# Kernel optimization log

Measured on AMD Instinct MI355X. Metric: run time of the kernel, lower is better.

Reference implementation:

```python
import jax, jax.numpy as jnp
import numpy as np

N_NODES = 50000
HIDDEN = 256
N_EDGES = 300000


def setup_inputs() -> dict:
    key = jax.random.key(0)
    k1, k2, k3, k4 = jax.random.split(key, 4)
    node_embeddings = jax.random.normal(k1, (N_NODES, HIDDEN), dtype=jnp.float32)
    edge_weights_index = jax.random.randint(k2, (2, N_EDGES), 0, N_NODES, dtype=jnp.int64)
    # lin1: Linear(2H -> H), lin2: Linear(H -> 1); jax convention [in, out]
    W1 = jax.random.normal(k3, (2 * HIDDEN, HIDDEN), dtype=jnp.float32) * (1.0 / np.sqrt(2 * HIDDEN))
    b1 = jnp.zeros((HIDDEN,), dtype=jnp.float32)
    W2 = jax.random.normal(k4, (HIDDEN, 1), dtype=jnp.float32) * (1.0 / np.sqrt(HIDDEN))
    b2 = jnp.zeros((1,), dtype=jnp.float32)
    return {"node_embeddings": node_embeddings, "edge_weights_index": edge_weights_index,
            "W1": W1, "b1": b1, "W2": W2, "b2": b2}


def reference(node_embeddings, edge_weights_index, W1, b1, W2, b2):
    src = edge_weights_index[0, :]
    trg = edge_weights_index[1, :]
    # Split W1 into src/trg halves: concat([s, t]) @ W1 == s @ W1s + t @ W1t.
    # Avoids materializing the [E, 2H] concatenated edge tensor.
    W1s, W1t = W1[:HIDDEN], W1[HIDDEN:]
    h = node_embeddings[src] @ W1s + node_embeddings[trg] @ W1t + b1  # [E, H]
    h = jax.nn.relu(h)
    prediction = h @ W2 + b2  # [E, 1]
    return prediction.reshape(-1)
```

## Files before the change

kernel.cpp:

```cpp
#include <hip/hip_runtime.h>
#include <hip/hip_bf16.h>

#define N_NODES 50000
#define HID     256
#define N_EDGES 300000
#define NT      32
#define NTILES  ((N_NODES + NT - 1) / NT)

typedef __attribute__((ext_vector_type(8))) short bf16x8;
typedef __attribute__((ext_vector_type(4))) float f32x4;

__device__ __forceinline__ unsigned short f2bf(float f) {
  unsigned int u = __float_as_uint(f);
  u = (u + 0x7FFFu + ((u >> 16) & 1u)) >> 16;
  return (unsigned short)u;
}
__device__ __forceinline__ float bflo(unsigned int u) { return __uint_as_float(u << 16); }
__device__ __forceinline__ float bfhi(unsigned int u) { return __uint_as_float(u & 0xFFFF0000u); }

__device__ __forceinline__ bf16x8 cvt8(float4 u, float4 v) {
  bf16x8 r;
  r[0] = (short)f2bf(u.x); r[1] = (short)f2bf(u.y);
  r[2] = (short)f2bf(u.z); r[3] = (short)f2bf(u.w);
  r[4] = (short)f2bf(v.x); r[5] = (short)f2bf(v.y);
  r[6] = (short)f2bf(v.z); r[7] = (short)f2bf(v.w);
  return r;
}

struct StageRegs { float4 a, b, c, d; };

__device__ __forceinline__ void load_tile(const float* __restrict__ E, int tile,
                                          int srow, int sg, StageRegs& s) {
  int grow = tile * NT + srow;
  if (grow < N_NODES) {
    const float4* p = reinterpret_cast<const float4*>(E + (size_t)grow * HID + sg * 8);
    s.a = p[0]; s.b = p[1]; s.c = p[32]; s.d = p[33];
  } else {
    s.a = s.b = s.c = s.d = make_float4(0.f, 0.f, 0.f, 0.f);
  }
}

__global__ __launch_bounds__(128) void pack_w_kernel(
    const float* __restrict__ W1, unsigned short* __restrict__ Wtf) {
  int k = blockIdx.x;
  int t = threadIdx.x;
  int half = t >> 6;
  int jj = (t & 63) * 4;
  const float4 v = *reinterpret_cast<const float4*>(
      W1 + (size_t)(half ? (HID + k) : k) * HID + jj);
  float vv[4] = {v.x, v.y, v.z, v.w};
#pragma unroll
  for (int e = 0; e < 4; ++e) {
    int j = half * HID + jj + e;
    int f    = (j >> 4) * 8 + (k >> 5);
    int lane = (j & 15) | (((k >> 3) & 3) << 4);
    int elem = k & 7;
    Wtf[f * 512 + lane * 8 + elem] = f2bf(vv[e]);
  }
}

__global__ __launch_bounds__(512, 2) void gemm_kernel(
    const float* __restrict__ E, const unsigned short* __restrict__ Wtf,
    const float* __restrict__ b1, unsigned short* __restrict__ P) {
  __shared__ alignas(16) char lds0[16384];
  __shared__ alignas(16) char lds1[16384];
  const int tid  = threadIdx.x;
  const int lane = tid & 63;
  const int w    = tid >> 6;

  bf16x8 a[4][8];
#pragma unroll
  for (int m = 0; m < 4; ++m)
#pragma unroll
    for (int kk = 0; kk < 8; ++kk)
      a[m][kk] = *reinterpret_cast<const bf16x8*>(
          Wtf + (((size_t)(w * 4 + m) * 8 + kk) << 9) + lane * 8);

  float4 bv[4];
#pragma unroll
  for (int m = 0; m < 4; ++m) {
    int fm = w * 4 + m;
    bv[m] = (fm < 16) ? *reinterpret_cast<const float4*>(b1 + fm * 16 + ((lane >> 4) << 2))
                      : make_float4(0.f, 0.f, 0.f, 0.f);
  }

  const int srow = tid >> 4;
  const int sg   = tid & 15;
  const int woff0 = srow * 512 + ((sg * 16) ^ ((srow & 7) << 4));
  const int woff1 = srow * 512 + (((sg + 16) * 16) ^ ((srow & 7) << 4));
  const int G = gridDim.x;

  auto write_tile = [&](char* buf, const StageRegs& s) {
    *reinterpret_cast<bf16x8*>(&buf[woff0]) = cvt8(s.a, s.b);
    *reinterpret_cast<bf16x8*>(&buf[woff1]) = cvt8(s.c, s.d);
  };

  auto compute_store = [&](const char* buf, int tt) {
    f32x4 acc[4][2] = {};
#pragma unroll
    for (int n = 0; n < 2; ++n) {
      int r   = n * 16 + (lane & 15);
      int rb  = r * 512;
      int sw  = (r & 7) << 4;
      int kb0 = (lane >> 4) << 4;
      bf16x8 bfr[8];
#pragma unroll
      for (int kk = 0; kk < 8; ++kk)
        bfr[kk] = *reinterpret_cast<const bf16x8*>(&buf[rb + ((kk * 64 + kb0) ^ sw)]);
#pragma unroll
      for (int kk = 0; kk < 8; ++kk)
#pragma unroll
        for (int m = 0; m < 4; ++m)
          acc[m][n] = __builtin_amdgcn_mfma_f32_16x16x32_bf16(a[m][kk], bfr[kk], acc[m][n], 0, 0, 0);
    }
#pragma unroll
    for (int m = 0; m < 4; ++m) {
      int pcb = (w * 4 + m) * 16 + ((lane >> 4) << 2);
#pragma unroll
      for (int n = 0; n < 2; ++n) {
        int node = tt * NT + n * 16 + (lane & 15);
        if (node < N_NODES) {
          ushort4 o;
          o.x = f2bf(acc[m][n][0] + bv[m].x);
          o.y = f2bf(acc[m][n][1] + bv[m].y);
          o.z = f2bf(acc[m][n][2] + bv[m].z);
          o.w = f2bf(acc[m][n][3] + bv[m].w);
          *reinterpret_cast<ushort4*>(P + (size_t)node * 512 + pcb) = o;
        }
      }
    }
  };

  int t = blockIdx.x;
  if (t >= NTILES) return;
  StageRegs sX, sY;
  load_tile(E, t, srow, sg, sX);
  if (t + G < NTILES) load_tile(E, t + G, srow, sg, sY);
  write_tile(lds0, sX);
  if (t + 2 * G < NTILES) load_tile(E, t + 2 * G, srow, sg, sX);
  __syncthreads();

  while (true) {
    if (t + G < NTILES) {
      write_tile(lds1, sY);
      if (t + 3 * G < NTILES) load_tile(E, t + 3 * G, srow, sg, sY);
    }
    compute_store(lds0, t);
    if (t + G >= NTILES) break;
    __syncthreads();
    t += G;
    if (t + G < NTILES) {
      write_tile(lds0, sX);
      if (t + 3 * G < NTILES) load_tile(E, t + 3 * G, srow, sg, sX);
    }
    compute_store(lds1, t);
    if (t + G >= NTILES) break;
    __syncthreads();
    t += G;
  }
}

__global__ __launch_bounds__(256) void edge_kernel(
    const int* __restrict__ idx, const unsigned short* __restrict__ P,
    const float* __restrict__ W2, const float* __restrict__ b2,
    float* __restrict__ out) {
  const int tid  = threadIdx.x;
  const int lane = tid & 63;
  const int l32  = lane & 31;
  const int half = lane >> 5;
  const int wv     = blockIdx.x * 4 + (tid >> 6);
  const int nwaves = gridDim.x * 4;
  const float4 w0 = *reinterpret_cast<const float4*>(W2 + l32 * 8);
  const float4 w1 = *reinterpret_cast<const float4*>(W2 + l32 * 8 + 4);
  const float bias = b2[0];
  for (int ep = wv; ep < N_EDGES / 2; ep += nwaves) {
    int e = ep * 2 + half;
    int s = idx[e];
    int t = idx[N_EDGES + e];
    uint4 ua = *reinterpret_cast<const uint4*>(P + (size_t)s * 512 + l32 * 8);
    uint4 ub = *reinterpret_cast<const uint4*>(P + (size_t)t * 512 + 256 + l32 * 8);
    float h0 = fmaxf(bflo(ua.x) + bflo(ub.x), 0.f);
    float h1 = fmaxf(bfhi(ua.x) + bfhi(ub.x), 0.f);
    float h2 = fmaxf(bflo(ua.y) + bflo(ub.y), 0.f);
    float h3 = fmaxf(bfhi(ua.y) + bfhi(ub.y), 0.f);
    float h4 = fmaxf(bflo(ua.z) + bflo(ub.z), 0.f);
    float h5 = fmaxf(bfhi(ua.z) + bfhi(ub.z), 0.f);
    float h6 = fmaxf(bflo(ua.w) + bflo(ub.w), 0.f);
    float h7 = fmaxf(bfhi(ua.w) + bfhi(ub.w), 0.f);
    float acc = h0 * w0.x + h1 * w0.y + h2 * w0.z + h3 * w0.w
              + h4 * w1.x + h5 * w1.y + h6 * w1.z + h7 * w1.w;
#pragma unroll
    for (int off = 1; off < 32; off <<= 1)
      acc += __shfl_xor(acc, off, 64);
    if (l32 == 0) out[e] = acc + bias;
  }
}

extern "C" void kernel_launch(void* const* d_in, const int* in_sizes, int n_in,
                              void* d_out, int out_size, void* d_ws, size_t ws_size,
                              hipStream_t stream) {
  const float* E   = (const float*)d_in[0];
  const int*   idx = (const int*)d_in[1];
  const float* W1  = (const float*)d_in[2];
  const float* b1  = (const float*)d_in[3];
  const float* W2  = (const float*)d_in[4];
  const float* b2  = (const float*)d_in[5];
  float* out = (float*)d_out;

  unsigned short* Wtf = (unsigned short*)d_ws;
  unsigned short* P   = (unsigned short*)((char*)d_ws + 262144);

  hipLaunchKernelGGL(pack_w_kernel, dim3(HID), dim3(128), 0, stream, W1, Wtf);
  hipLaunchKernelGGL(gemm_kernel, dim3(256), dim3(512), 0, stream, E, Wtf, b1, P);
  hipLaunchKernelGGL(edge_kernel, dim3(2048), dim3(256), 0, stream, idx, P, W2, b2, out);
}
```

Baseline: 78.54 us.

## Bucket edges by source node range to improve gather locality in edge kernel

Adds a three-kernel counting sort (histogram, scan, scatter) that bins edges by the high bits of the source node index and writes permuted (src, trg, edge id) records. A new edge kernel walks the sorted list with a swizzled block-to-chunk mapping so that source-row gathers from P hit nearby rows and reuse cache. The cost is three extra launches, a 300k-record scatter with atomics, and scattered output writes; it falls back to the old path if the workspace is too small.

```diff
diff --git a/kernel.cpp b/kernel.cpp
--- a/kernel.cpp
+++ b/kernel.cpp
@@ -6,6 +6,11 @@
 #define N_EDGES 300000
 #define NT      32
 #define NTILES  ((N_NODES + NT - 1) / NT)
+#define NBINS   64
+#define SBLK    128
+#define CHUNK   ((N_EDGES + SBLK - 1) / SBLK)
+#define EBLK    1024
+#define EPB     ((N_EDGES + EBLK - 1) / EBLK)
 
 typedef __attribute__((ext_vector_type(8))) short bf16x8;
 typedef __attribute__((ext_vector_type(4))) float f32x4;
@@ -56,6 +61,53 @@
     int lane = (j & 15) | (((k >> 3) & 3) << 4);
     int elem = k & 7;
     Wtf[f * 512 + lane * 8 + elem] = f2bf(vv[e]);
+  }
+}
+
+__global__ __launch_bounds__(256) void hist_kernel(const int* __restrict__ idx,
+                                                   int* __restrict__ blockhist) {
+  __shared__ int h[NBINS];
+  for (int i = threadIdx.x; i < NBINS; i += 256) h[i] = 0;
+  __syncthreads();
+  int b = blockIdx.x;
+  int lo = b * CHUNK, hi = min(lo + CHUNK, N_EDGES);
+  for (int e = lo + threadIdx.x; e < hi; e += 256)
+    atomicAdd(&h[idx[e] >> 10], 1);
+  __syncthreads();
+  for (int i = threadIdx.x; i < NBINS; i += 256)
+    blockhist[b * NBINS + i] = h[i];
+}
+
+__global__ __launch_bounds__(64) void scan_kernel(const int* __restrict__ blockhist,
+                                                  int* __restrict__ base2) {
+  int bin = threadIdx.x;
+  int tot = 0;
+  for (int b = 0; b < SBLK; ++b) tot += blockhist[b * NBINS + bin];
+  int incl = tot;
+#pragma unroll
+  for (int off = 1; off < 64; off <<= 1) {
+    int v = __shfl_up(incl, off, 64);
+    if (bin >= off) incl += v;
+  }
+  int run = incl - tot;
+  for (int b = 0; b < SBLK; ++b) {
+    base2[b * NBINS + bin] = run;
+    run += blockhist[b * NBINS + bin];
+  }
+}
+
+__global__ __launch_bounds__(256) void scatter_kernel(const int* __restrict__ idx,
+                                                      const int* __restrict__ base2,
+                                                      int4* __restrict__ eperm) {
+  __shared__ int cur[NBINS];
+  int b = blockIdx.x;
+  for (int i = threadIdx.x; i < NBINS; i += 256) cur[i] = base2[b * NBINS + i];
+  __syncthreads();
+  int lo = b * CHUNK, hi = min(lo + CHUNK, N_EDGES);
+  for (int e = lo + threadIdx.x; e < hi; e += 256) {
+    int s = idx[e], t = idx[N_EDGES + e];
+    int pos = atomicAdd(&cur[s >> 10], 1);
+    eperm[pos] = make_int4(s, t, e, 0);
   }
 }
 
@@ -157,6 +209,42 @@
     if (t + G >= NTILES) break;
     __syncthreads();
     t += G;
+  }
+}
+
+__global__ __launch_bounds__(256) void edge_sorted_kernel(
+    const int4* __restrict__ eperm, const unsigned short* __restrict__ P,
+    const float* __restrict__ W2, const float* __restrict__ b2,
+    float* __restrict__ out) {
+  const int tid  = threadIdx.x;
+  const int lane = tid & 63;
+  const int l32  = lane & 31;
+  const int half = lane >> 5;
+  const int swz  = ((blockIdx.x & 7) << 7) + (blockIdx.x >> 3);
+  const int start = swz * EPB;
+  const int end   = min(start + EPB, N_EDGES);
+  const int hid   = (tid >> 6) * 2 + half;
+  const float4 w0 = *reinterpret_cast<const float4*>(W2 + l32 * 8);
+  const float4 w1 = *reinterpret_cast<const float4*>(W2 + l32 * 8 + 4);
+  const float bias = b2[0];
+  for (int i = start + hid; i < end; i += 8) {
+    int4 q = eperm[i];
+    uint4 ua = *reinterpret_cast<const uint4*>(P + (size_t)q.x * 512 + l32 * 8);
+    uint4 ub = *reinterpret_cast<const uint4*>(P + (size_t)q.y * 512 + 256 + l32 * 8);
+    float h0 = fmaxf(bflo(ua.x) + bflo(ub.x), 0.f);
+    float h1 = fmaxf(bfhi(ua.x) + bfhi(ub.x), 0.f);
+    float h2 = fmaxf(bflo(ua.y) + bflo(ub.y), 0.f);
+    float h3 = fmaxf(bfhi(ua.y) + bfhi(ub.y), 0.f);
+    float h4 = fmaxf(bflo(ua.z) + bflo(ub.z), 0.f);
+    float h5 = fmaxf(bfhi(ua.z) + bfhi(ub.z), 0.f);
+    float h6 = fmaxf(bflo(ua.w) + bflo(ub.w), 0.f);
+    float h7 = fmaxf(bfhi(ua.w) + bfhi(ub.w), 0.f);
+    float acc = h0 * w0.x + h1 * w0.y + h2 * w0.z + h3 * w0.w
+              + h4 * w1.x + h5 * w1.y + h6 * w1.z + h7 * w1.w;
+#pragma unroll
+    for (int off = 1; off < 32; off <<= 1)
+      acc += __shfl_xor(acc, off, 64);
+    if (l32 == 0) out[q.z] = acc + bias;
   }
 }
 
@@ -207,10 +295,25 @@
   const float* b2  = (const float*)d_in[5];
   float* out = (float*)d_out;
 
-  unsigned short* Wtf = (unsigned short*)d_ws;
-  unsigned short* P   = (unsigned short*)((char*)d_ws + 262144);
+  char* ws = (char*)d_ws;
+  unsigned short* Wtf = (unsigned short*)ws;
+  unsigned short* P   = (unsigned short*)(ws + 262144);
+  size_t off = 262144 + 51200000;
+  int*  blockhist = (int*)(ws + off);
+  int*  base2     = (int*)(ws + off + 32768);
+  int4* eperm     = (int4*)(ws + off + 65536);
+  size_t need = off + 65536 + (size_t)(EBLK * EPB) * 16;
 
   hipLaunchKernelGGL(pack_w_kernel, dim3(HID), dim3(128), 0, stream, W1, Wtf);
-  hipLaunchKernelGGL(gemm_kernel, dim3(256), dim3(512), 0, stream, E, Wtf, b1, P);
-  hipLaunchKernelGGL(edge_kernel, dim3(2048), dim3(256), 0, stream, idx, P, W2, b2, out);
-}
+  if (ws_size >= need) {
+    hipLaunchKernelGGL(hist_kernel, dim3(SBLK), dim3(256), 0, stream, idx, blockhist);
+    hipLaunchKernelGGL(scan_kernel, dim3(1), dim3(64), 0, stream, blockhist, base2);
+    hipLaunchKernelGGL(scatter_kernel, dim3(SBLK), dim3(256), 0, stream, idx, base2, eperm);
+    hipLaunchKernelGGL(gemm_kernel, dim3(256), dim3(512), 0, stream, E, Wtf, b1, P);
+    hipLaunchKernelGGL(edge_sorted_kernel, dim3(EBLK), dim3(256), 0, stream,
+                       eperm, P, W2, b2, out);
+  } else {
+    hipLaunchKernelGGL(gemm_kernel, dim3(256), dim3(512), 0, stream, E, Wtf, b1, P);
+    hipLaunchKernelGGL(edge_kernel, dim3(2048), dim3(256), 0, stream, idx, P, W2, b2, out);
+  }
+}
```

New measurement: 102.4 us. 30.3% more time.
